# Optimization experiments

Hardware: AMD Instinct MI355X
Metric: run time of the kernel (lower is better)

The kernel has to match this reference:

```python
import jax, jax.numpy as jnp
import numpy as np

EPS = 1e-8

def _l2norm(x):
    return x / (jnp.linalg.norm(x, axis=-1, keepdims=True) + EPS)

def setup_inputs() -> dict:
    key = jax.random.key(0)
    k1, k2, k3, k4, k5, k6 = jax.random.split(key, 6)
    NQ, NB, NF = 16384, 128, 64
    HD = 2 * NF
    Q = jax.random.normal(k1, (NQ, HD), dtype=jnp.float32)
    reference_angles = jax.random.uniform(k2, (NF,), dtype=jnp.float32) * 2.0 * np.pi
    probes = jax.random.normal(k3, (NB, HD), dtype=jnp.float32)
    # params: perturb around the torch inits (log(e-1), zeros, zeros) for a non-degenerate test
    init_val = float(np.log(np.e - 1.0))
    q_weights_raw = init_val + 0.1 * jax.random.normal(k4, (NB, NF), dtype=jnp.float32)
    q_magnitude_weights = 0.1 * jax.random.normal(k5, (NB, NF), dtype=jnp.float32)
    q_bias = 0.1 * jax.random.normal(k6, (NB,), dtype=jnp.float32)
    return {"Q": Q, "reference_angles": reference_angles, "probes": probes,
            "q_weights_raw": q_weights_raw, "q_magnitude_weights": q_magnitude_weights,
            "q_bias": q_bias}

def reference(Q, reference_angles, probes, q_weights_raw, q_magnitude_weights, q_bias):
    NF = reference_angles.shape[0]
    # --- shared probe layer: L2 normalize then RoPE-rotate (front/back real/imag layout)
    pn = _l2norm(probes)                      # (B, 2F)
    pr, pi = pn[:, :NF], pn[:, NF:]
    c, s = jnp.cos(reference_angles), jnp.sin(reference_angles)
    P_real = pr * c - pi * s                  # (B, F)
    P_imag = pr * s + pi * c
    # --- distance-based scorer
    Qn = _l2norm(Q)                           # (Nq, 2F)
    Q_real, Q_imag = Qn[:, :NF], Qn[:, NF:]
    err_r = P_real[None, :, :] - Q_real[:, None, :]   # (Nq, B, F)
    err_i = P_imag[None, :, :] - Q_imag[:, None, :]
    distance = jnp.sqrt(err_r ** 2 + err_i ** 2 + EPS)
    eff_w = -jax.nn.softplus(q_weights_raw)           # (B, F), negative weights
    distance_term = jnp.einsum('qbf,bf->qb', distance, eff_w)
    Q_mag = jnp.sqrt(Q_real ** 2 + Q_imag ** 2 + EPS)  # (Nq, F)
    magnitude_term = Q_mag @ q_magnitude_weights.T     # (Nq, B)
    return distance_term + magnitude_term + q_bias
```

## Files before the change

kernel.cpp:

```cpp
#include <hip/hip_runtime.h>

#define NQ 16384
#define NB 128
#define NF 64
#define HD 128
#define EPSF 1e-8f
#define BTILE 8
#define NBT (NB / BTILE)

struct FRow {
    float4 d[BTILE];
    float  m[BTILE];
};

__global__ __launch_bounds__(256) void prep_kernel(
    const float* __restrict__ Q,
    const float* __restrict__ probes,
    const float* __restrict__ angles,
    const float* __restrict__ qw,
    const float* __restrict__ mw,
    float4* __restrict__ qvals,
    FRow* __restrict__ tab) {
    if (blockIdx.x < 2048) {
        const int q  = blockIdx.x * 8 + (threadIdx.x >> 5);
        const int sl = threadIdx.x & 31;
        const float2* Q2 = (const float2*)Q;
        float2 a = Q2[q * 64 + sl];
        float2 c = Q2[q * 64 + 32 + sl];
        float ss = a.x * a.x + a.y * a.y + c.x * c.x + c.y * c.y;
        #pragma unroll
        for (int m = 1; m < 32; m <<= 1) ss += __shfl_xor(ss, m);
        float inv = 1.0f / (sqrtf(ss) + EPSF);
        float Qr0 = a.x * inv, Qr1 = a.y * inv;
        float Qi0 = c.x * inv, Qi1 = c.y * inv;
        float B0 = Qr0 * Qr0 + Qi0 * Qi0;
        float B1 = Qr1 * Qr1 + Qi1 * Qi1;
        qvals[(size_t)q * NF + 2 * sl]     = make_float4(Qr0, Qi0, B0, sqrtf(B0 + EPSF));
        qvals[(size_t)q * NF + 2 * sl + 1] = make_float4(Qr1, Qi1, B1, sqrtf(B1 + EPSF));
    } else {
        const int b    = (blockIdx.x - 2048) * 4 + (threadIdx.x >> 6);
        const int lane = threadIdx.x & 63;
        float p0 = probes[b * HD + lane];
        float p1 = probes[b * HD + 64 + lane];
        float ss = p0 * p0 + p1 * p1;
        #pragma unroll
        for (int m = 1; m < 64; m <<= 1) ss += __shfl_xor(ss, m);
        float inv = 1.0f / (sqrtf(ss) + EPSF);
        float pr = p0 * inv, pi = p1 * inv;
        float ang = angles[lane];
        float cc = cosf(ang), sn = sinf(ang);
        float Pr = pr * cc - pi * sn;
        float Pi = pr * sn + pi * cc;
        float x = qw[b * NF + lane];
        float sp = (x > 0.0f) ? (x + log1pf(expf(-x))) : log1pf(expf(x));
        FRow* r = &tab[(b >> 3) * NF + lane];
        r->d[b & 7] = make_float4(-2.0f * Pr, -2.0f * Pi, Pr * Pr + Pi * Pi + EPSF, -sp);
        r->m[b & 7] = mw[b * NF + lane];
    }
}

__global__ __launch_bounds__(256, 4) void main_kernel(
    const FRow* __restrict__ tab,
    const float4* __restrict__ qvals,
    const float* __restrict__ bias,
    float* __restrict__ out) {
    const int bt   = blockIdx.x & (NBT - 1);
    const int qblk = blockIdx.x / NBT;
    const int q = qblk * 256 + (threadIdx.x >> 6) * 64 + (threadIdx.x & 63);

    const FRow* __restrict__ tr = tab + bt * NF;
    const float4* __restrict__ qp = qvals + (size_t)q * NF;

    float acc[BTILE];
    #pragma unroll
    for (int i = 0; i < BTILE; ++i) acc[i] = 0.0f;

    #pragma unroll 4
    for (int f = 0; f < NF; ++f) {
        float4 qv = qp[f];
        #pragma unroll
        for (int bb = 0; bb < BTILE; ++bb) {
            float4 td = tr[f].d[bb];
            float tm  = tr[f].m[bb];
            float t = td.z + qv.z;
            t = fmaf(td.y, qv.y, t);
            t = fmaf(td.x, qv.x, t);
            t = fmaxf(t, 0.0f);
            float d = __builtin_amdgcn_sqrtf(t);
            acc[bb] = fmaf(td.w, d, acc[bb]);
            acc[bb] = fmaf(tm, qv.w, acc[bb]);
        }
    }

    #pragma unroll
    for (int bb = 0; bb < BTILE; ++bb) acc[bb] += bias[bt * BTILE + bb];
    float* op = out + (size_t)q * NB + bt * BTILE;
    *(float4*)op       = make_float4(acc[0], acc[1], acc[2], acc[3]);
    *(float4*)(op + 4) = make_float4(acc[4], acc[5], acc[6], acc[7]);
}

extern "C" void kernel_launch(void* const* d_in, const int* in_sizes, int n_in,
                              void* d_out, int out_size, void* d_ws, size_t ws_size,
                              hipStream_t stream) {
    const float* Q      = (const float*)d_in[0];
    const float* angles = (const float*)d_in[1];
    const float* probes = (const float*)d_in[2];
    const float* qw     = (const float*)d_in[3];
    const float* mw     = (const float*)d_in[4];
    const float* bias   = (const float*)d_in[5];
    float* out = (float*)d_out;

    char* ws = (char*)d_ws;
    FRow*   tab   = (FRow*)ws;
    float4* qvals = (float4*)(ws + NBT * NF * sizeof(FRow));

    prep_kernel<<<2048 + NB / 4, 256, 0, stream>>>(Q, probes, angles, qw, mw, qvals, tab);
    main_kernel<<<(NQ / 256) * NBT, 256, 0, stream>>>(tab, qvals, bias, out);
}
```

Baseline: 111.1 us.

## Pack feature pairs for packed-FP32 math with coalesced feature-major query layout

Query precomputed values move to a feature-pair-major layout (transposed through shared memory in prep), so consecutive threads read consecutive addresses instead of striding by 64 float4s. The probe table is reorganized into two-wide vectors so the inner loop uses packed two-element FMAs over feature pairs. The main kernel also prefetches the next pair's query data and remaps block indices so blocks sharing query rows land on the same XCD for L2 reuse. The cost is a shared-memory transpose and a __syncthreads in prep, plus more registers per thread. The clamp on negative values changes from max(t,0) to fabs.

```diff
diff --git a/kernel.cpp b/kernel.cpp
--- a/kernel.cpp
+++ b/kernel.cpp
@@ -7,10 +7,17 @@
 #define EPSF 1e-8f
 #define BTILE 8
 #define NBT (NB / BTILE)
+#define NFP (NF / 2)
 
-struct FRow {
-    float4 d[BTILE];
-    float  m[BTILE];
+typedef float f32x2 __attribute__((ext_vector_type(2)));
+typedef float f32x4 __attribute__((ext_vector_type(4)));
+
+struct FP2Row {
+    f32x2 x2[BTILE];
+    f32x2 y2[BTILE];
+    f32x2 z2[BTILE];
+    f32x2 w2[BTILE];
+    f32x2 m2[BTILE];
 };
 
 __global__ __launch_bounds__(256) void prep_kernel(
@@ -19,11 +26,15 @@
     const float* __restrict__ angles,
     const float* __restrict__ qw,
     const float* __restrict__ mw,
-    float4* __restrict__ qvals,
-    FRow* __restrict__ tab) {
+    f32x4* __restrict__ qA,
+    f32x4* __restrict__ qB,
+    FP2Row* __restrict__ tab) {
+    __shared__ f32x4 sA[8][NFP + 1];
+    __shared__ f32x4 sB[8][NFP + 1];
     if (blockIdx.x < 2048) {
-        const int q  = blockIdx.x * 8 + (threadIdx.x >> 5);
+        const int qi = threadIdx.x >> 5;
         const int sl = threadIdx.x & 31;
+        const int q  = blockIdx.x * 8 + qi;
         const float2* Q2 = (const float2*)Q;
         float2 a = Q2[q * 64 + sl];
         float2 c = Q2[q * 64 + 32 + sl];
@@ -35,68 +46,95 @@
         float Qi0 = c.x * inv, Qi1 = c.y * inv;
         float B0 = Qr0 * Qr0 + Qi0 * Qi0;
         float B1 = Qr1 * Qr1 + Qi1 * Qi1;
-        qvals[(size_t)q * NF + 2 * sl]     = make_float4(Qr0, Qi0, B0, sqrtf(B0 + EPSF));
-        qvals[(size_t)q * NF + 2 * sl + 1] = make_float4(Qr1, Qi1, B1, sqrtf(B1 + EPSF));
+        f32x4 Av; Av.x = Qr0; Av.y = Qr1; Av.z = Qi0; Av.w = Qi1;
+        f32x4 Bv; Bv.x = B0;  Bv.y = B1;
+        Bv.z = sqrtf(B0 + EPSF); Bv.w = sqrtf(B1 + EPSF);
+        sA[qi][sl] = Av;
+        sB[qi][sl] = Bv;
+        __syncthreads();
+        const int sl2 = threadIdx.x >> 3;
+        const int qi2 = threadIdx.x & 7;
+        const int qb  = blockIdx.x * 8;
+        qA[sl2 * NQ + qb + qi2] = sA[qi2][sl2];
+        qB[sl2 * NQ + qb + qi2] = sB[qi2][sl2];
     } else {
-        const int b    = (blockIdx.x - 2048) * 4 + (threadIdx.x >> 6);
-        const int lane = threadIdx.x & 63;
-        float p0 = probes[b * HD + lane];
-        float p1 = probes[b * HD + 64 + lane];
+        const int b = (blockIdx.x - 2048) * 4 + (threadIdx.x >> 6);
+        const int f = threadIdx.x & 63;
+        float p0 = probes[b * HD + f];
+        float p1 = probes[b * HD + 64 + f];
         float ss = p0 * p0 + p1 * p1;
         #pragma unroll
         for (int m = 1; m < 64; m <<= 1) ss += __shfl_xor(ss, m);
         float inv = 1.0f / (sqrtf(ss) + EPSF);
         float pr = p0 * inv, pi = p1 * inv;
-        float ang = angles[lane];
+        float ang = angles[f];
         float cc = cosf(ang), sn = sinf(ang);
         float Pr = pr * cc - pi * sn;
         float Pi = pr * sn + pi * cc;
-        float x = qw[b * NF + lane];
+        float x = qw[b * NF + f];
         float sp = (x > 0.0f) ? (x + log1pf(expf(-x))) : log1pf(expf(x));
-        FRow* r = &tab[(b >> 3) * NF + lane];
-        r->d[b & 7] = make_float4(-2.0f * Pr, -2.0f * Pi, Pr * Pr + Pi * Pi + EPSF, -sp);
-        r->m[b & 7] = mw[b * NF + lane];
+        FP2Row* r = &tab[(b >> 3) * NFP + (f >> 1)];
+        const int h  = f & 1;
+        const int bb = b & 7;
+        ((float*)&r->x2[bb])[h] = -2.0f * Pr;
+        ((float*)&r->y2[bb])[h] = -2.0f * Pi;
+        ((float*)&r->z2[bb])[h] = Pr * Pr + Pi * Pi + EPSF;
+        ((float*)&r->w2[bb])[h] = -sp;
+        ((float*)&r->m2[bb])[h] = mw[b * NF + f];
     }
 }
 
 __global__ __launch_bounds__(256, 4) void main_kernel(
-    const FRow* __restrict__ tab,
-    const float4* __restrict__ qvals,
+    const FP2Row* __restrict__ tab,
+    const f32x4* __restrict__ qA,
+    const f32x4* __restrict__ qB,
     const float* __restrict__ bias,
     float* __restrict__ out) {
-    const int bt   = blockIdx.x & (NBT - 1);
-    const int qblk = blockIdx.x / NBT;
-    const int q = qblk * 256 + (threadIdx.x >> 6) * 64 + (threadIdx.x & 63);
+    const int p    = blockIdx.x;
+    const int xcd  = p & 7;
+    const int j    = p >> 3;
+    const int qblk = xcd * 8 + (j >> 4);
+    const int bt   = j & 15;
+    const int q    = qblk * 256 + threadIdx.x;
 
-    const FRow* __restrict__ tr = tab + bt * NF;
-    const float4* __restrict__ qp = qvals + (size_t)q * NF;
+    const FP2Row* __restrict__ tr = tab + bt * NFP;
 
-    float acc[BTILE];
+    f32x2 acc[BTILE];
     #pragma unroll
     for (int i = 0; i < BTILE; ++i) acc[i] = 0.0f;
 
-    #pragma unroll 4
-    for (int f = 0; f < NF; ++f) {
-        float4 qv = qp[f];
+    f32x4 A = qA[q];
+    f32x4 B = qB[q];
+    for (int fp = 0; fp < NFP; ++fp) {
+        const int fpn = (fp < NFP - 1) ? fp + 1 : fp;
+        f32x4 An = qA[fpn * NQ + q];
+        f32x4 Bn = qB[fpn * NQ + q];
+        f32x2 qr2 = __builtin_shufflevector(A, A, 0, 1);
+        f32x2 qi2 = __builtin_shufflevector(A, A, 2, 3);
+        f32x2 qz2 = __builtin_shufflevector(B, B, 0, 1);
+        f32x2 qm2 = __builtin_shufflevector(B, B, 2, 3);
+        const FP2Row* r = tr + fp;
         #pragma unroll
         for (int bb = 0; bb < BTILE; ++bb) {
-            float4 td = tr[f].d[bb];
-            float tm  = tr[f].m[bb];
-            float t = td.z + qv.z;
-            t = fmaf(td.y, qv.y, t);
-            t = fmaf(td.x, qv.x, t);
-            t = fmaxf(t, 0.0f);
-            float d = __builtin_amdgcn_sqrtf(t);
-            acc[bb] = fmaf(td.w, d, acc[bb]);
-            acc[bb] = fmaf(tm, qv.w, acc[bb]);
+            f32x2 t = r->z2[bb] + qz2;
+            t = __builtin_elementwise_fma(r->y2[bb], qi2, t);
+            t = __builtin_elementwise_fma(r->x2[bb], qr2, t);
+            f32x2 d;
+            d.x = __builtin_amdgcn_sqrtf(__builtin_fabsf(t.x));
+            d.y = __builtin_amdgcn_sqrtf(__builtin_fabsf(t.y));
+            acc[bb] = __builtin_elementwise_fma(r->w2[bb], d, acc[bb]);
+            acc[bb] = __builtin_elementwise_fma(r->m2[bb], qm2, acc[bb]);
         }
+        A = An; B = Bn;
     }
 
+    float o[BTILE];
     #pragma unroll
-    for (int bb = 0; bb < BTILE; ++bb) acc[bb] += bias[bt * BTILE + bb];
+    for (int bb = 0; bb < BTILE; ++bb)
+        o[bb] = acc[bb].x + acc[bb].y + bias[bt * BTILE + bb];
     float* op = out + (size_t)q * NB + bt * BTILE;
-    *(float4*)op       = make_float4(acc[0], acc[1], acc[2], acc[3]);
-    *(float4*)(op + 4) = make_float4(acc[4], acc[5], acc[6], acc[7]);
+    *(float4*)op       = make_float4(o[0], o[1], o[2], o[3]);
+    *(float4*)(op + 4) = make_float4(o[4], o[5], o[6], o[7]);
 }
 
 extern "C" void kernel_launch(void* const* d_in, const int* in_sizes, int n_in,
@@ -111,9 +149,10 @@
     float* out = (float*)d_out;
 
     char* ws = (char*)d_ws;
-    FRow*   tab   = (FRow*)ws;
-    float4* qvals = (float4*)(ws + NBT * NF * sizeof(FRow));
+    FP2Row* tab = (FP2Row*)ws;
+    f32x4*  qA  = (f32x4*)(ws + NBT * NFP * sizeof(FP2Row));
+    f32x4*  qB  = qA + (size_t)NFP * NQ;
 
-    prep_kernel<<<2048 + NB / 4, 256, 0, stream>>>(Q, probes, angles, qw, mw, qvals, tab);
-    main_kernel<<<(NQ / 256) * NBT, 256, 0, stream>>>(tab, qvals, bias, out);
+    prep_kernel<<<2048 + NB / 4, 256, 0, stream>>>(Q, probes, angles, qw, mw, qA, qB, tab);
+    main_kernel<<<(NQ / 256) * NBT, 256, 0, stream>>>(tab, qA, qB, bias, out);
 }
```

Result: faster. 100.9 us (-9.3%).
